# Kernel optimization log

Measured on AMD Instinct MI355X. Metric: run time of the kernel, lower is better.

The kernel has to match this reference:

```python
import jax, jax.numpy as jnp
import numpy as np

N, E, F_IN, H, C = 10000, 640000, 128, 128, 40


def setup_inputs() -> dict:
    key = jax.random.key(0)
    ks = jax.random.split(key, 8)
    x = jax.random.normal(ks[0], (N, F_IN), dtype=jnp.float32)
    edge_index = jax.random.randint(ks[1], (2, E), 0, N, dtype=jnp.int64)
    W1 = jax.random.normal(ks[2], (F_IN, H), dtype=jnp.float32) / np.sqrt(F_IN)
    b1 = jnp.zeros((H,), dtype=jnp.float32)
    W2 = jax.random.normal(ks[3], (H, H), dtype=jnp.float32) / np.sqrt(H)
    b2 = jnp.zeros((H,), dtype=jnp.float32)
    Wc = jax.random.normal(ks[4], (H, C), dtype=jnp.float32) / np.sqrt(H)
    bc = jnp.zeros((C,), dtype=jnp.float32)
    return {"x": x, "edge_index": edge_index, "W1": W1, "b1": b1,
            "W2": W2, "b2": b2, "Wc": Wc, "bc": bc}


def _gcn_conv(x, src, dst, norm, W, b):
    # GCNConv: out = D^{-1/2}(A+I)D^{-1/2} (x @ W) + b
    h = x @ W                               # [N, H]
    msg = h[src] * norm[:, None]            # gather + per-edge normalize
    out = jax.ops.segment_sum(msg, dst, num_segments=N)  # scatter-add
    return out + b


def reference(x, edge_index, W1, b1, W2, b2, Wc, bc):
    # add self-loops (as PyG GCNConv does by default)
    loops = jnp.arange(N, dtype=edge_index.dtype)
    src = jnp.concatenate([edge_index[0], loops])   # [E+N]
    dst = jnp.concatenate([edge_index[1], loops])   # [E+N]
    # symmetric normalization deg^{-1/2} with self-loops included
    deg = jax.ops.segment_sum(jnp.ones_like(dst, dtype=x.dtype), dst, num_segments=N)
    dinv = jax.lax.rsqrt(deg)                       # deg >= 1 due to self-loops
    norm = dinv[src] * dinv[dst]                    # [E+N]

    h = _gcn_conv(x, src, dst, norm, W1, b1)
    h = jax.nn.relu(h)
    h = _gcn_conv(h, src, dst, norm, W2, b2)
    logits = h @ Wc + bc                            # [N, C]
    return jax.nn.log_softmax(logits, axis=1)
```

## Files before the change

kernel.cpp:

```cpp
#include <hip/hip_runtime.h>
#include <hip/hip_fp16.h>
#include <math.h>

#define FDIM 128
#define CDIM 40
#define DMAX 192
#define NMAX 10240
#define SLICE_SHIFT 14
#define SLICE_SZ (1 << SLICE_SHIFT)

__device__ __forceinline__ uint2 pack_half4(float4 v) {
    __half2 p0 = __float22half2_rn(make_float2(v.x, v.y));
    __half2 p1 = __float22half2_rn(make_float2(v.z, v.w));
    uint2 u;
    u.x = *(unsigned int*)&p0;
    u.y = *(unsigned int*)&p1;
    return u;
}

__device__ __forceinline__ void upadd(float& a0, float& a1, unsigned int u) {
    __half2 h = *(__half2*)&u;
    float2 f = __half22float2(h);
    a0 += f.x; a1 += f.y;
}

__global__ __launch_bounds__(1024) void k_hist(
        const int* __restrict__ dst, unsigned short* __restrict__ lrank,
        int* __restrict__ cnt, int e, int n) {
    __shared__ int h[NMAX];
    int tid = threadIdx.x;
    for (int i = tid; i < n; i += 1024) h[i] = 0;
    __syncthreads();
    int base = (int)blockIdx.x << SLICE_SHIFT;
    int end = base + SLICE_SZ; if (end > e) end = e;
    for (int i = base + tid * 4; i < end; i += 4096) {
        if (i + 3 < end) {
            int4 d = *(const int4*)(dst + i);
            int p0 = atomicAdd(&h[d.x], 1);
            int p1 = atomicAdd(&h[d.y], 1);
            int p2 = atomicAdd(&h[d.z], 1);
            int p3 = atomicAdd(&h[d.w], 1);
            ushort4 r;
            r.x = (unsigned short)p0; r.y = (unsigned short)p1;
            r.z = (unsigned short)p2; r.w = (unsigned short)p3;
            *(ushort4*)(lrank + i) = r;
        } else {
            for (int k = i; k < end; ++k)
                lrank[k] = (unsigned short)atomicAdd(&h[dst[k]], 1);
        }
    }
    __syncthreads();
    int* c = cnt + (size_t)blockIdx.x * n;
    for (int i = tid; i < n; i += 1024) c[i] = h[i];
}

__global__ __launch_bounds__(256) void k_scan_wc(
        int* __restrict__ cnt, int* __restrict__ deg, int nslice, int n,
        int scanB, const float* __restrict__ W2, const float* __restrict__ Wc,
        const float* __restrict__ b2, const float* __restrict__ bc,
        float* __restrict__ W2c, float* __restrict__ bias2c) {
    int tid = threadIdx.x;
    if ((int)blockIdx.x < scanB) {
        int v = blockIdx.x * 256 + tid;
        if (v >= n) return;
        int s = 0;
        for (int b = 0; b < nslice; ++b) {
            int t = cnt[(size_t)b * n + v];
            cnt[(size_t)b * n + v] = s;
            s += t;
        }
        deg[v] = s;
    } else {
        int o = ((int)blockIdx.x - scanB) * 256 + tid;
        if (o >= FDIM * CDIM) return;
        int k = o / CDIM, c = o - k * CDIM;
        float acc = 0.f;
        for (int j = 0; j < FDIM; ++j)
            acc += W2[k * FDIM + j] * Wc[j * CDIM + c];
        W2c[o] = acc;
        if (o < CDIM) {
            float b = bc[o];
            for (int j = 0; j < FDIM; ++j)
                b += b2[j] * Wc[j * CDIM + o];
            bias2c[o] = b;
        }
    }
}

__global__ __launch_bounds__(256) void k_mega(
        const float* __restrict__ A, const float* __restrict__ W,
        const int* __restrict__ deg, uint2* __restrict__ h16, int n,
        const int* __restrict__ src, const int* __restrict__ dst,
        const unsigned short* __restrict__ lrank, const int* __restrict__ base,
        unsigned short* __restrict__ col, int e, int gemm_blocks) {
    __shared__ float As[32][FDIM];
    int tid = threadIdx.x;
    if ((int)blockIdx.x < gemm_blocks) {
        int r0 = blockIdx.x * 32;
        for (int t = tid; t < 32 * 32; t += 256) {
            int r = t >> 5, c4 = t & 31;
            int gr = r0 + r;
            float4 v = make_float4(0.f, 0.f, 0.f, 0.f);
            if (gr < n) v = ((const float4*)A)[(size_t)gr * 32 + c4];
            ((float4*)As[r])[c4] = v;
        }
        __syncthreads();
        int cb = (tid & 31) * 4;
        int rb = (tid >> 5) * 4;
        float4 acc0 = make_float4(0,0,0,0), acc1 = acc0, acc2 = acc0, acc3 = acc0;
        for (int k = 0; k < FDIM; ++k) {
            float4 w = *(const float4*)(W + k * FDIM + cb);
            float a0 = As[rb + 0][k], a1 = As[rb + 1][k];
            float a2 = As[rb + 2][k], a3 = As[rb + 3][k];
            acc0.x += a0 * w.x; acc0.y += a0 * w.y; acc0.z += a0 * w.z; acc0.w += a0 * w.w;
            acc1.x += a1 * w.x; acc1.y += a1 * w.y; acc1.z += a1 * w.z; acc1.w += a1 * w.w;
            acc2.x += a2 * w.x; acc2.y += a2 * w.y; acc2.z += a2 * w.z; acc2.w += a2 * w.w;
            acc3.x += a3 * w.x; acc3.y += a3 * w.y; acc3.z += a3 * w.z; acc3.w += a3 * w.w;
        }
        float4 accs[4] = {acc0, acc1, acc2, acc3};
        #pragma unroll
        for (int i = 0; i < 4; ++i) {
            int gr = r0 + rb + i;
            if (gr < n) {
                float dinv = rsqrtf((float)(deg[gr] + 1));
                float4 v = accs[i];
                v.x *= dinv; v.y *= dinv; v.z *= dinv; v.w *= dinv;
                h16[(size_t)gr * 32 + (cb >> 2)] = pack_half4(v);
            }
        }
    } else {
        int g = ((int)blockIdx.x - gemm_blocks) * 256 + tid;
        int i4 = g * 4;
        if (i4 + 3 < e) {
            const int* bs = base + (size_t)(i4 >> SLICE_SHIFT) * n;
            int4 d = ((const int4*)dst)[g];
            int4 s = ((const int4*)src)[g];
            ushort4 lr = ((const ushort4*)lrank)[g];
            int p0 = bs[d.x] + lr.x;
            int p1 = bs[d.y] + lr.y;
            int p2 = bs[d.z] + lr.z;
            int p3 = bs[d.w] + lr.w;
            if (p0 < DMAX) col[(size_t)d.x * DMAX + p0] = (unsigned short)s.x;
            if (p1 < DMAX) col[(size_t)d.y * DMAX + p1] = (unsigned short)s.y;
            if (p2 < DMAX) col[(size_t)d.z * DMAX + p2] = (unsigned short)s.z;
            if (p3 < DMAX) col[(size_t)d.w * DMAX + p3] = (unsigned short)s.w;
        } else if (i4 < e) {
            for (int k = i4; k < e; ++k) {
                int d = dst[k];
                int p = base[(size_t)(k >> SLICE_SHIFT) * n + d] + lrank[k];
                if (p < DMAX) col[(size_t)d * DMAX + p] = (unsigned short)src[k];
            }
        }
    }
}

__device__ __forceinline__ void wave_gather(
        float& o0, float& o1, const unsigned int* __restrict__ hs,
        const unsigned short* __restrict__ col, int node, int dn, int lane) {
    float a0 = 0.f, a1 = 0.f, b0 = 0.f, b1 = 0.f;
    upadd(a0, a1, hs[(size_t)node * 64 + lane]);
    const uint4* cl8 = (const uint4*)(col + (size_t)node * DMAX);
    int j = 0;
    for (; j + 16 <= dn; j += 16) {
        uint4 cA = cl8[(j >> 3)];
        uint4 cB = cl8[(j >> 3) + 1];
        int s0 = cA.x & 0xFFFF, s1 = cA.x >> 16;
        int s2 = cA.y & 0xFFFF, s3 = cA.y >> 16;
        int s4 = cA.z & 0xFFFF, s5 = cA.z >> 16;
        int s6 = cA.w & 0xFFFF, s7 = cA.w >> 16;
        int s8 = cB.x & 0xFFFF, s9 = cB.x >> 16;
        int sa = cB.y & 0xFFFF, sb = cB.y >> 16;
        int sc = cB.z & 0xFFFF, sd = cB.z >> 16;
        int se = cB.w & 0xFFFF, sf = cB.w >> 16;
        unsigned int q0 = hs[(size_t)s0 * 64 + lane];
        unsigned int q1 = hs[(size_t)s1 * 64 + lane];
        unsigned int q2 = hs[(size_t)s2 * 64 + lane];
        unsigned int q3 = hs[(size_t)s3 * 64 + lane];
        unsigned int q4 = hs[(size_t)s4 * 64 + lane];
        unsigned int q5 = hs[(size_t)s5 * 64 + lane];
        unsigned int q6 = hs[(size_t)s6 * 64 + lane];
        unsigned int q7 = hs[(size_t)s7 * 64 + lane];
        unsigned int q8 = hs[(size_t)s8 * 64 + lane];
        unsigned int q9 = hs[(size_t)s9 * 64 + lane];
        unsigned int qa = hs[(size_t)sa * 64 + lane];
        unsigned int qb = hs[(size_t)sb * 64 + lane];
        unsigned int qc = hs[(size_t)sc * 64 + lane];
        unsigned int qd = hs[(size_t)sd * 64 + lane];
        unsigned int qe = hs[(size_t)se * 64 + lane];
        unsigned int qf = hs[(size_t)sf * 64 + lane];
        upadd(a0, a1, q0); upadd(b0, b1, q1);
        upadd(a0, a1, q2); upadd(b0, b1, q3);
        upadd(a0, a1, q4); upadd(b0, b1, q5);
        upadd(a0, a1, q6); upadd(b0, b1, q7);
        upadd(a0, a1, q8); upadd(b0, b1, q9);
        upadd(a0, a1, qa); upadd(b0, b1, qb);
        upadd(a0, a1, qc); upadd(b0, b1, qd);
        upadd(a0, a1, qe); upadd(b0, b1, qf);
    }
    for (; j + 8 <= dn; j += 8) {
        uint4 c = cl8[j >> 3];
        int s0 = c.x & 0xFFFF, s1 = c.x >> 16;
        int s2 = c.y & 0xFFFF, s3 = c.y >> 16;
        int s4 = c.z & 0xFFFF, s5 = c.z >> 16;
        int s6 = c.w & 0xFFFF, s7 = c.w >> 16;
        unsigned int q0 = hs[(size_t)s0 * 64 + lane];
        unsigned int q1 = hs[(size_t)s1 * 64 + lane];
        unsigned int q2 = hs[(size_t)s2 * 64 + lane];
        unsigned int q3 = hs[(size_t)s3 * 64 + lane];
        unsigned int q4 = hs[(size_t)s4 * 64 + lane];
        unsigned int q5 = hs[(size_t)s5 * 64 + lane];
        unsigned int q6 = hs[(size_t)s6 * 64 + lane];
        unsigned int q7 = hs[(size_t)s7 * 64 + lane];
        upadd(a0, a1, q0); upadd(b0, b1, q1);
        upadd(a0, a1, q2); upadd(b0, b1, q3);
        upadd(a0, a1, q4); upadd(b0, b1, q5);
        upadd(a0, a1, q6); upadd(b0, b1, q7);
    }
    const unsigned short* cl = col + (size_t)node * DMAX;
    for (; j < dn; ++j) upadd(a0, a1, hs[(size_t)cl[j] * 64 + lane]);
    o0 = a0 + b0;
    o1 = a1 + b1;
}

__global__ __launch_bounds__(512) void k_agg1(
        const unsigned int* __restrict__ hs1, const unsigned short* __restrict__ col,
        const int* __restrict__ deg, const float* __restrict__ b1,
        float* __restrict__ a1, int n) {
    int node = (blockIdx.x * 512 + threadIdx.x) >> 6;
    int lane = threadIdx.x & 63;
    if (node >= n) return;
    int dn = deg[node];
    float dinv = rsqrtf((float)(dn + 1));
    if (dn > DMAX) dn = DMAX;
    float o0, o1;
    wave_gather(o0, o1, hs1, col, node, dn, lane);
    float2 bb = ((const float2*)b1)[lane];
    float v0 = fmaxf(dinv * o0 + bb.x, 0.f);
    float v1 = fmaxf(dinv * o1 + bb.y, 0.f);
    ((float2*)a1)[(size_t)node * 64 + lane] = make_float2(v0, v1);
}

__global__ __launch_bounds__(320) void k_gemm2c(
        const float* __restrict__ A, const float* __restrict__ W2c,
        const int* __restrict__ deg, float* __restrict__ z, int n) {
    __shared__ float As[32][FDIM];
    __shared__ float Ws[FDIM * CDIM];
    int tid = threadIdx.x;
    int r0 = blockIdx.x * 32;
    for (int t = tid; t < 32 * 32; t += 320) {
        int r = t >> 5, c4 = t & 31;
        int gr = r0 + r;
        float4 v = make_float4(0.f, 0.f, 0.f, 0.f);
        if (gr < n) v = ((const float4*)A)[(size_t)gr * 32 + c4];
        ((float4*)As[r])[c4] = v;
    }
    for (int t = tid; t < FDIM * CDIM; t += 320) Ws[t] = W2c[t];
    __syncthreads();
    int c = tid % CDIM;
    int g = tid / CDIM;
    int rb = g * 4;
    float acc0 = 0.f, acc1 = 0.f, acc2 = 0.f, acc3 = 0.f;
    for (int k = 0; k < FDIM; ++k) {
        float w = Ws[k * CDIM + c];
        acc0 += As[rb + 0][k] * w;
        acc1 += As[rb + 1][k] * w;
        acc2 += As[rb + 2][k] * w;
        acc3 += As[rb + 3][k] * w;
    }
    float accs[4] = {acc0, acc1, acc2, acc3};
    #pragma unroll
    for (int i = 0; i < 4; ++i) {
        int gr = r0 + rb + i;
        if (gr < n) {
            float dinv = rsqrtf((float)(deg[gr] + 1));
            z[(size_t)gr * CDIM + c] = dinv * accs[i];
        }
    }
}

__global__ __launch_bounds__(512) void k_agg2s(
        const float* __restrict__ z, const unsigned short* __restrict__ col,
        const int* __restrict__ deg, const float* __restrict__ bias2c,
        float* __restrict__ out, int n) {
    int tid = threadIdx.x;
    int wv = tid >> 6, lane = tid & 63;
    int node = blockIdx.x * 8 + wv;
    if (node >= n) return;
    int dn = deg[node];
    float dinv = rsqrtf((float)(dn + 1));
    if (dn > DMAX) dn = DMAX;
    const uint4* cl8 = (const uint4*)(col + (size_t)node * DMAX);
    float a = z[(size_t)node * CDIM + lane];
    float b = 0.f;
    int j = 0;
    for (; j + 16 <= dn; j += 16) {
        uint4 cA = cl8[(j >> 3)];
        uint4 cB = cl8[(j >> 3) + 1];
        int s0 = cA.x & 0xFFFF, s1 = cA.x >> 16;
        int s2 = cA.y & 0xFFFF, s3 = cA.y >> 16;
        int s4 = cA.z & 0xFFFF, s5 = cA.z >> 16;
        int s6 = cA.w & 0xFFFF, s7 = cA.w >> 16;
        int s8 = cB.x & 0xFFFF, s9 = cB.x >> 16;
        int sa = cB.y & 0xFFFF, sb = cB.y >> 16;
        int sc = cB.z & 0xFFFF, sd = cB.z >> 16;
        int se = cB.w & 0xFFFF, sf = cB.w >> 16;
        float q0 = z[(size_t)s0 * CDIM + lane];
        float q1 = z[(size_t)s1 * CDIM + lane];
        float q2 = z[(size_t)s2 * CDIM + lane];
        float q3 = z[(size_t)s3 * CDIM + lane];
        float q4 = z[(size_t)s4 * CDIM + lane];
        float q5 = z[(size_t)s5 * CDIM + lane];
        float q6 = z[(size_t)s6 * CDIM + lane];
        float q7 = z[(size_t)s7 * CDIM + lane];
        float q8 = z[(size_t)s8 * CDIM + lane];
        float q9 = z[(size_t)s9 * CDIM + lane];
        float qa = z[(size_t)sa * CDIM + lane];
        float qb = z[(size_t)sb * CDIM + lane];
        float qc = z[(size_t)sc * CDIM + lane];
        float qd = z[(size_t)sd * CDIM + lane];
        float qe = z[(size_t)se * CDIM + lane];
        float qf = z[(size_t)sf * CDIM + lane];
        a += q0; b += q1; a += q2; b += q3;
        a += q4; b += q5; a += q6; b += q7;
        a += q8; b += q9; a += qa; b += qb;
        a += qc; b += qd; a += qe; b += qf;
    }
    for (; j + 8 <= dn; j += 8) {
        uint4 c = cl8[j >> 3];
        int s0 = c.x & 0xFFFF, s1 = c.x >> 16;
        int s2 = c.y & 0xFFFF, s3 = c.y >> 16;
        int s4 = c.z & 0xFFFF, s5 = c.z >> 16;
        int s6 = c.w & 0xFFFF, s7 = c.w >> 16;
        float q0 = z[(size_t)s0 * CDIM + lane];
        float q1 = z[(size_t)s1 * CDIM + lane];
        float q2 = z[(size_t)s2 * CDIM + lane];
        float q3 = z[(size_t)s3 * CDIM + lane];
        float q4 = z[(size_t)s4 * CDIM + lane];
        float q5 = z[(size_t)s5 * CDIM + lane];
        float q6 = z[(size_t)s6 * CDIM + lane];
        float q7 = z[(size_t)s7 * CDIM + lane];
        a += q0; b += q1; a += q2; b += q3;
        a += q4; b += q5; a += q6; b += q7;
    }
    const unsigned short* cl = col + (size_t)node * DMAX;
    for (; j < dn; ++j) a += z[(size_t)cl[j] * CDIM + lane];
    float lv = (lane < CDIM) ? (dinv * (a + b) + bias2c[lane]) : -INFINITY;
    float m = lv;
    for (int off = 32; off > 0; off >>= 1) m = fmaxf(m, __shfl_down(m, off));
    m = __shfl(m, 0);
    float e = (lane < CDIM) ? expf(lv - m) : 0.0f;
    float s = e;
    for (int off = 32; off > 0; off >>= 1) s += __shfl_down(s, off);
    s = __shfl(s, 0);
    if (lane < CDIM) out[(size_t)node * CDIM + lane] = lv - m - logf(s);
}


extern "C" void kernel_launch(void* const* d_in, const int* in_sizes, int n_in,
                              void* d_out, int out_size, void* d_ws, size_t ws_size,
                              hipStream_t stream) {
    const float* x  = (const float*)d_in[0];
    const int*   ei = (const int*)d_in[1];
    const float* W1 = (const float*)d_in[2];
    const float* b1 = (const float*)d_in[3];
    const float* W2 = (const float*)d_in[4];
    const float* b2 = (const float*)d_in[5];
    const float* Wc = (const float*)d_in[6];
    const float* bc = (const float*)d_in[7];
    float* out = (float*)d_out;

    const int N = in_sizes[0] / FDIM;
    const int E = in_sizes[1] / 2;
    const int* srcp = ei;
    const int* dstp = ei + E;
    const int NSLICE = (E + SLICE_SZ - 1) >> SLICE_SHIFT;

    char* ws = (char*)d_ws;
    auto alloc = [&](size_t bytes) {
        char* p = ws;
        ws += (bytes + 255) & ~(size_t)255;
        return p;
    };
    int*            deg    = (int*)           alloc((size_t)N * 4);
    int*            cnt    = (int*)           alloc((size_t)NSLICE * N * 4);
    unsigned short* lrank  = (unsigned short*)alloc((size_t)E * 2);
    unsigned short* col    = (unsigned short*)alloc((size_t)N * DMAX * 2);
    uint4*          h1h    = (uint4*)         alloc((size_t)N * 256);
    float*          a1     = (float*)         alloc((size_t)N * FDIM * 4);
    float*          W2c    = (float*)         alloc((size_t)FDIM * CDIM * 4);
    float*          bias2c = (float*)         alloc((size_t)CDIM * 4);
    float*          z      = (float*)         alloc((size_t)N * CDIM * 4 + 256);

    k_hist<<<NSLICE, 1024, 0, stream>>>(dstp, lrank, cnt, E, N);

    int scanB = (N + 255) / 256;
    int wcB = (FDIM * CDIM + 255) / 256;
    k_scan_wc<<<scanB + wcB, 256, 0, stream>>>(
        cnt, deg, NSLICE, N, scanB, W2, Wc, b2, bc, W2c, bias2c);

    int gb = (N + 31) / 32;
    int fb = (E / 4 + 255) / 256;
    k_mega<<<gb + fb, 256, 0, stream>>>(
        x, W1, deg, (uint2*)h1h, N, srcp, dstp, lrank, cnt, col, E, gb);

    k_agg1<<<((size_t)N * 64 + 511) / 512, 512, 0, stream>>>(
        (const unsigned int*)h1h, col, deg, b1, a1, N);

    k_gemm2c<<<(N + 31) / 32, 320, 0, stream>>>(a1, W2c, deg, z, N);

    k_agg2s<<<(N + 7) / 8, 512, 0, stream>>>(z, col, deg, bias2c, out, N);
}
```

Baseline: 148.2 us.

## Fuse layer-1 aggregation with the 128x40 projection GEMM into one kernel

Merges the layer-1 gather/ReLU kernel with the following projection by W2c, so each wave writes its aggregated row to shared memory and immediately computes the 40-wide projection. This removes the a1 intermediate buffer and its global write and re-read, plus one kernel launch. In exchange, every 8-node block reloads the full 20 KB W2c into LDS and the per-row GEMM leaves 24 of 64 lanes idle. The layer-2 gather also clamps lanes past 40 to valid columns, so those lanes no longer read past each z row.

```diff
diff --git a/kernel.cpp b/kernel.cpp
--- a/kernel.cpp
+++ b/kernel.cpp
@@ -222,60 +222,39 @@
     o1 = a1 + b1;
 }
 
-__global__ __launch_bounds__(512) void k_agg1(
+__global__ __launch_bounds__(512) void k_agg1f(
         const unsigned int* __restrict__ hs1, const unsigned short* __restrict__ col,
         const int* __restrict__ deg, const float* __restrict__ b1,
-        float* __restrict__ a1, int n) {
-    int node = (blockIdx.x * 512 + threadIdx.x) >> 6;
-    int lane = threadIdx.x & 63;
+        const float* __restrict__ W2c, float* __restrict__ z, int n) {
+    __shared__ float Ws[FDIM * CDIM];
+    __shared__ float As[8][FDIM];
+    int tid = threadIdx.x;
+    for (int t = tid; t < FDIM * CDIM; t += 512) Ws[t] = W2c[t];
+    __syncthreads();
+    int wv = tid >> 6, lane = tid & 63;
+    int node = blockIdx.x * 8 + wv;
     if (node >= n) return;
     int dn = deg[node];
     float dinv = rsqrtf((float)(dn + 1));
-    if (dn > DMAX) dn = DMAX;
+    int dnc = dn > DMAX ? DMAX : dn;
     float o0, o1;
-    wave_gather(o0, o1, hs1, col, node, dn, lane);
+    wave_gather(o0, o1, hs1, col, node, dnc, lane);
     float2 bb = ((const float2*)b1)[lane];
     float v0 = fmaxf(dinv * o0 + bb.x, 0.f);
     float v1 = fmaxf(dinv * o1 + bb.y, 0.f);
-    ((float2*)a1)[(size_t)node * 64 + lane] = make_float2(v0, v1);
-}
-
-__global__ __launch_bounds__(320) void k_gemm2c(
-        const float* __restrict__ A, const float* __restrict__ W2c,
-        const int* __restrict__ deg, float* __restrict__ z, int n) {
-    __shared__ float As[32][FDIM];
-    __shared__ float Ws[FDIM * CDIM];
-    int tid = threadIdx.x;
-    int r0 = blockIdx.x * 32;
-    for (int t = tid; t < 32 * 32; t += 320) {
-        int r = t >> 5, c4 = t & 31;
-        int gr = r0 + r;
-        float4 v = make_float4(0.f, 0.f, 0.f, 0.f);
-        if (gr < n) v = ((const float4*)A)[(size_t)gr * 32 + c4];
-        ((float4*)As[r])[c4] = v;
-    }
-    for (int t = tid; t < FDIM * CDIM; t += 320) Ws[t] = W2c[t];
-    __syncthreads();
-    int c = tid % CDIM;
-    int g = tid / CDIM;
-    int rb = g * 4;
-    float acc0 = 0.f, acc1 = 0.f, acc2 = 0.f, acc3 = 0.f;
-    for (int k = 0; k < FDIM; ++k) {
-        float w = Ws[k * CDIM + c];
-        acc0 += As[rb + 0][k] * w;
-        acc1 += As[rb + 1][k] * w;
-        acc2 += As[rb + 2][k] * w;
-        acc3 += As[rb + 3][k] * w;
-    }
-    float accs[4] = {acc0, acc1, acc2, acc3};
-    #pragma unroll
-    for (int i = 0; i < 4; ++i) {
-        int gr = r0 + rb + i;
-        if (gr < n) {
-            float dinv = rsqrtf((float)(deg[gr] + 1));
-            z[(size_t)gr * CDIM + c] = dinv * accs[i];
-        }
-    }
+    ((float2*)As[wv])[lane] = make_float2(v0, v1);
+    int c = (lane < CDIM) ? lane : 0;
+    const float* row = As[wv];
+    float acc = 0.f;
+    for (int k = 0; k < FDIM; k += 4) {
+        float a0 = row[k + 0], a1 = row[k + 1];
+        float a2 = row[k + 2], a3 = row[k + 3];
+        acc += a0 * Ws[(k + 0) * CDIM + c];
+        acc += a1 * Ws[(k + 1) * CDIM + c];
+        acc += a2 * Ws[(k + 2) * CDIM + c];
+        acc += a3 * Ws[(k + 3) * CDIM + c];
+    }
+    if (lane < CDIM) z[(size_t)node * CDIM + lane] = dinv * acc;
 }
 
 __global__ __launch_bounds__(512) void k_agg2s(
@@ -289,8 +268,9 @@
     int dn = deg[node];
     float dinv = rsqrtf((float)(dn + 1));
     if (dn > DMAX) dn = DMAX;
+    int cc = (lane < CDIM) ? lane : (lane - 24);
     const uint4* cl8 = (const uint4*)(col + (size_t)node * DMAX);
-    float a = z[(size_t)node * CDIM + lane];
+    float a = z[(size_t)node * CDIM + cc];
     float b = 0.f;
     int j = 0;
     for (; j + 16 <= dn; j += 16) {
@@ -304,22 +284,22 @@
         int sa = cB.y & 0xFFFF, sb = cB.y >> 16;
         int sc = cB.z & 0xFFFF, sd = cB.z >> 16;
         int se = cB.w & 0xFFFF, sf = cB.w >> 16;
-        float q0 = z[(size_t)s0 * CDIM + lane];
-        float q1 = z[(size_t)s1 * CDIM + lane];
-        float q2 = z[(size_t)s2 * CDIM + lane];
-        float q3 = z[(size_t)s3 * CDIM + lane];
-        float q4 = z[(size_t)s4 * CDIM + lane];
-        float q5 = z[(size_t)s5 * CDIM + lane];
-        float q6 = z[(size_t)s6 * CDIM + lane];
-        float q7 = z[(size_t)s7 * CDIM + lane];
-        float q8 = z[(size_t)s8 * CDIM + lane];
-        float q9 = z[(size_t)s9 * CDIM + lane];
-        float qa = z[(size_t)sa * CDIM + lane];
-        float qb = z[(size_t)sb * CDIM + lane];
-        float qc = z[(size_t)sc * CDIM + lane];
-        float qd = z[(size_t)sd * CDIM + lane];
-        float qe = z[(size_t)se * CDIM + lane];
-        float qf = z[(size_t)sf * CDIM + lane];
+        float q0 = z[(size_t)s0 * CDIM + cc];
+        float q1 = z[(size_t)s1 * CDIM + cc];
+        float q2 = z[(size_t)s2 * CDIM + cc];
+        float q3 = z[(size_t)s3 * CDIM + cc];
+        float q4 = z[(size_t)s4 * CDIM + cc];
+        float q5 = z[(size_t)s5 * CDIM + cc];
+        float q6 = z[(size_t)s6 * CDIM + cc];
+        float q7 = z[(size_t)s7 * CDIM + cc];
+        float q8 = z[(size_t)s8 * CDIM + cc];
+        float q9 = z[(size_t)s9 * CDIM + cc];
+        float qa = z[(size_t)sa * CDIM + cc];
+        float qb = z[(size_t)sb * CDIM + cc];
+        float qc = z[(size_t)sc * CDIM + cc];
+        float qd = z[(size_t)sd * CDIM + cc];
+        float qe = z[(size_t)se * CDIM + cc];
+        float qf = z[(size_t)sf * CDIM + cc];
         a += q0; b += q1; a += q2; b += q3;
         a += q4; b += q5; a += q6; b += q7;
         a += q8; b += q9; a += qa; b += qb;
@@ -331,19 +311,19 @@
         int s2 = c.y & 0xFFFF, s3 = c.y >> 16;
         int s4 = c.z & 0xFFFF, s5 = c.z >> 16;
         int s6 = c.w & 0xFFFF, s7 = c.w >> 16;
-        float q0 = z[(size_t)s0 * CDIM + lane];
-        float q1 = z[(size_t)s1 * CDIM + lane];
-        float q2 = z[(size_t)s2 * CDIM + lane];
-        float q3 = z[(size_t)s3 * CDIM + lane];
-        float q4 = z[(size_t)s4 * CDIM + lane];
-        float q5 = z[(size_t)s5 * CDIM + lane];
-        float q6 = z[(size_t)s6 * CDIM + lane];
-        float q7 = z[(size_t)s7 * CDIM + lane];
+        float q0 = z[(size_t)s0 * CDIM + cc];
+        float q1 = z[(size_t)s1 * CDIM + cc];
+        float q2 = z[(size_t)s2 * CDIM + cc];
+        float q3 = z[(size_t)s3 * CDIM + cc];
+        float q4 = z[(size_t)s4 * CDIM + cc];
+        float q5 = z[(size_t)s5 * CDIM + cc];
+        float q6 = z[(size_t)s6 * CDIM + cc];
+        float q7 = z[(size_t)s7 * CDIM + cc];
         a += q0; b += q1; a += q2; b += q3;
         a += q4; b += q5; a += q6; b += q7;
     }
     const unsigned short* cl = col + (size_t)node * DMAX;
-    for (; j < dn; ++j) a += z[(size_t)cl[j] * CDIM + lane];
+    for (; j < dn; ++j) a += z[(size_t)cl[j] * CDIM + cc];
     float lv = (lane < CDIM) ? (dinv * (a + b) + bias2c[lane]) : -INFINITY;
     float m = lv;
     for (int off = 32; off > 0; off >>= 1) m = fmaxf(m, __shfl_down(m, off));
@@ -386,7 +366,6 @@
     unsigned short* lrank  = (unsigned short*)alloc((size_t)E * 2);
     unsigned short* col    = (unsigned short*)alloc((size_t)N * DMAX * 2);
     uint4*          h1h    = (uint4*)         alloc((size_t)N * 256);
-    float*          a1     = (float*)         alloc((size_t)N * FDIM * 4);
     float*          W2c    = (float*)         alloc((size_t)FDIM * CDIM * 4);
     float*          bias2c = (float*)         alloc((size_t)CDIM * 4);
     float*          z      = (float*)         alloc((size_t)N * CDIM * 4 + 256);
@@ -403,10 +382,8 @@
     k_mega<<<gb + fb, 256, 0, stream>>>(
         x, W1, deg, (uint2*)h1h, N, srcp, dstp, lrank, cnt, col, E, gb);
 
-    k_agg1<<<((size_t)N * 64 + 511) / 512, 512, 0, stream>>>(
-        (const unsigned int*)h1h, col, deg, b1, a1, N);
-
-    k_gemm2c<<<(N + 31) / 32, 320, 0, stream>>>(a1, W2c, deg, z, N);
+    k_agg1f<<<(N + 7) / 8, 512, 0, stream>>>(
+        (const unsigned int*)h1h, col, deg, b1, W2c, z, N);
 
     k_agg2s<<<(N + 7) / 8, 512, 0, stream>>>(z, col, deg, bias2c, out, N);
 }
```

Result: faster. 141.6 us (-4.5%).
